# Performance work log

Measured on AMD Instinct MI355X. Metric: run time of the kernel, lower is better.

## Reference

```python
import jax, jax.numpy as jnp
import numpy as np
from jax import lax

N_WORDS = 8192
MAX_WLEN = 16
VOCAB = 500
EMB = 64
HID = 256
N_SENT = 256
SENT_LEN = 32  # N_SENT * SENT_LEN == N_WORDS (sentlens are uniform)


def setup_inputs() -> dict:
    key = jax.random.key(0)
    ks = jax.random.split(key, 12)
    chars = jax.random.randint(ks[0], (N_WORDS, MAX_WLEN), 1, VOCAB, dtype=jnp.int32)
    # packed LSTM requires lengths sorted descending
    wordlens = jnp.sort(jax.random.randint(ks[1], (N_WORDS,), 1, MAX_WLEN + 1, dtype=jnp.int32))[::-1]
    # permutation mapping sorted order -> original order (tensor_unsort input)
    word_orig_idx = jax.random.permutation(ks[2], N_WORDS).astype(jnp.int32)
    emb_table = (jax.random.normal(ks[3], (VOCAB, EMB), dtype=jnp.float32) * 0.1).at[0].set(0.0)  # padding_idx=0
    W_ih = jax.random.normal(ks[4], (4 * HID, EMB), dtype=jnp.float32) * 0.05
    W_hh = jax.random.normal(ks[5], (4 * HID, HID), dtype=jnp.float32) * 0.05
    b_ih = jax.random.normal(ks[6], (4 * HID,), dtype=jnp.float32) * 0.02
    b_hh = jax.random.normal(ks[7], (4 * HID,), dtype=jnp.float32) * 0.02
    attn_w = jax.random.normal(ks[8], (HID,), dtype=jnp.float32) * 0.1  # char_attn weight (zero-init in orig; random for nontrivial test)
    h_init = jax.random.normal(ks[9], (HID,), dtype=jnp.float32) * 0.02  # charlstm_h_init (num_layers=1)
    c_init = jax.random.normal(ks[10], (HID,), dtype=jnp.float32) * 0.02
    return dict(chars=chars, wordlens=wordlens, word_orig_idx=word_orig_idx,
                emb_table=emb_table, W_ih=W_ih, W_hh=W_hh, b_ih=b_ih, b_hh=b_hh,
                attn_w=attn_w, h_init=h_init, c_init=c_init)


def _char_model(chars, wordlens, word_orig_idx, emb_table, W_ih, W_hh, b_ih, b_hh, attn_w, h_init, c_init):
    n = chars.shape[0]
    pad_mask = jnp.arange(MAX_WLEN)[None, :] >= wordlens[:, None]  # [N,L] True where padded
    embs = emb_table[chars]  # [N,L,E] (dropout is identity at eval)

    def step(carry, x_t):
        h, c = carry
        gates = x_t @ W_ih.T + h @ W_hh.T + (b_ih + b_hh)  # [N,4H]
        i, f, g, o = jnp.split(gates, 4, axis=-1)  # torch gate order i,f,g,o
        c = jax.nn.sigmoid(f) * c + jax.nn.sigmoid(i) * jnp.tanh(g)
        h = jax.nn.sigmoid(o) * jnp.tanh(c)
        return (h, c), h

    h0 = jnp.broadcast_to(h_init, (n, HID))
    c0 = jnp.broadcast_to(c_init, (n, HID))
    _, hs = lax.scan(step, (h0, c0), embs.transpose(1, 0, 2))  # hs: [L,N,H]
    char_reps = hs.transpose(1, 0, 2)  # [N,L,H]
    # pad_packed_sequence yields zeros at padded positions
    char_reps = jnp.where(pad_mask[..., None], 0.0, char_reps)
    # masked sigmoid attention pool: weights.bmm(char_reps)
    w = jax.nn.sigmoid(char_reps @ attn_w)  # [N,L]
    w = jnp.where(pad_mask, 0.0, w)
    res = jnp.einsum('nl,nlh->nh', w, char_reps)  # [N,H]
    # tensor_unsort: restore original word order
    res = jnp.zeros_like(res).at[word_orig_idx].set(res)
    # split(sentlens) + pack + pad_packed with uniform sentlens -> reshape
    return res.reshape(N_SENT, SENT_LEN, HID)


def reference(chars, wordlens, word_orig_idx, emb_table, W_ih, W_hh, b_ih, b_hh, attn_w, h_init, c_init):
    return _char_model(chars, wordlens, word_orig_idx, emb_table, W_ih, W_hh, b_ih, b_hh, attn_w, h_init, c_init)
```

## Files before the change

kernel.cpp:

```cpp
#include <hip/hip_runtime.h>
#include <math.h>

#define HID 256
#define EMB 64
#define KTOT 320
#define MT 32
#define NWORDS 8192
#define NBLK (NWORDS / MT)
#define THREADS 512
#define KT 10
#define XSTR 328
#define GSTR 40

typedef _Float16 f16;
typedef _Float16 f16x8 __attribute__((ext_vector_type(8)));
typedef _Float16 f16x4 __attribute__((ext_vector_type(4)));
typedef float f32x4 __attribute__((ext_vector_type(4)));

__device__ __forceinline__ float sigm(float x) { return 1.0f / (1.0f + __expf(-x)); }

__global__ __launch_bounds__(KTOT) void prep_w(const float* __restrict__ W_ih,
                                               const float* __restrict__ W_hh,
                                               const float* __restrict__ b_ih,
                                               const float* __restrict__ b_hh,
                                               f16* __restrict__ Wfrag,
                                               float* __restrict__ bias) {
  const int g = blockIdx.x;
  const int k = threadIdx.x;
  const float w = (k < HID) ? W_hh[g * HID + k] : W_ih[g * EMB + (k - HID)];
  const int kt = k >> 5;
  Wfrag[(size_t)(kt * 1024 + g) * 32 + (k & 31)] = (f16)w;
  if (k == 0) bias[g] = b_ih[g] + b_hh[g];
}

__global__ __launch_bounds__(THREADS, 2) void lstm_mfma(
    const int* __restrict__ chars, const int* __restrict__ wordlens,
    const int* __restrict__ orig_idx, const float* __restrict__ emb_table,
    const float* __restrict__ attn_w, const float* __restrict__ h_init,
    const float* __restrict__ c_init, const f16* __restrict__ Wfrag,
    const float* __restrict__ bias, float* __restrict__ out) {
  __shared__ __align__(16) f16 Xs[MT * XSTR];
  __shared__ __align__(16) f16 gatesS[1024 * GSTR];
  __shared__ int   chars_s[MT * 16];
  __shared__ float part_s[8 * 16];
  __shared__ float wgt_s[MT];
  __shared__ int   len_s[MT];
  __shared__ int   oidx_s[MT];

  const int tid  = threadIdx.x;
  const int w0   = blockIdx.x * MT;
  const int j    = tid & 255;
  const int mh   = tid >> 8;
  const int lane = tid & 63;
  const int wv   = tid >> 6;
  const int r15  = lane & 15, c4 = lane >> 4;
  const int n0   = wv * 128;

  chars_s[tid] = chars[w0 * 16 + tid];
  if (tid < MT) { len_s[tid] = wordlens[w0 + tid]; oidx_s[tid] = orig_idx[w0 + tid]; }

  const float aw   = attn_w[j];
  const float cini = c_init[j];
  const f16   hini = (f16)h_init[j];
#pragma unroll
  for (int mm = 0; mm < 16; ++mm) Xs[(mh * 16 + mm) * XSTR + j] = hini;

  float c_reg[16], res_acc[16], h_new[16];
#pragma unroll
  for (int mm = 0; mm < 16; ++mm) { c_reg[mm] = cini; res_acc[mm] = 0.0f; h_new[mm] = 0.0f; }

  float biasr[8];
#pragma unroll
  for (int ntl = 0; ntl < 8; ++ntl) biasr[ntl] = bias[n0 + ntl * 16 + r15];

  __syncthreads();
  int steps = 1;
#pragma unroll
  for (int m = 0; m < MT; ++m) steps = max(steps, len_s[m]);

  for (int t = 0; t < steps; ++t) {
    {
      const int m = tid >> 4, eg = tid & 15;
      const int ch = chars_s[m * 16 + t];
      const float4 e = ((const float4*)emb_table)[ch * 16 + eg];
      f16x4 ev = { (f16)e.x, (f16)e.y, (f16)e.z, (f16)e.w };
      *(f16x4*)&Xs[m * XSTR + HID + eg * 4] = ev;
    }
    __syncthreads();

    f32x4 acc[8][2];
#pragma unroll
    for (int ntl = 0; ntl < 8; ++ntl) {
      const f32x4 b4 = { biasr[ntl], biasr[ntl], biasr[ntl], biasr[ntl] };
      acc[ntl][0] = b4;
      acc[ntl][1] = b4;
    }

#pragma unroll 2
    for (int kt = 0; kt < KT; ++kt) {
      const f16x8 a0 = *(const f16x8*)&Xs[r15 * XSTR + kt * 32 + c4 * 8];
      const f16x8 a1 = *(const f16x8*)&Xs[(16 + r15) * XSTR + kt * 32 + c4 * 8];
      const f16x8* __restrict__ Wp = (const f16x8*)(Wfrag + (size_t)kt * 1024 * 32);
#pragma unroll
      for (int ntl = 0; ntl < 8; ++ntl) {
        const f16x8 b = Wp[(size_t)(n0 + ntl * 16 + r15) * 4 + c4];
        acc[ntl][0] = __builtin_amdgcn_mfma_f32_16x16x32_f16(a0, b, acc[ntl][0], 0, 0, 0);
        acc[ntl][1] = __builtin_amdgcn_mfma_f32_16x16x32_f16(a1, b, acc[ntl][1], 0, 0, 0);
      }
    }

#pragma unroll
    for (int ntl = 0; ntl < 8; ++ntl) {
      const int g = n0 + ntl * 16 + r15;
#pragma unroll
      for (int mt = 0; mt < 2; ++mt) {
        const f32x4 v = acc[ntl][mt];
        f16x4 hv = { (f16)v.x, (f16)v.y, (f16)v.z, (f16)v.w };
        *(f16x4*)&gatesS[g * GSTR + mt * 16 + c4 * 4] = hv;
      }
    }
    __syncthreads();

    f16x8 gA[4], gB[4];
#pragma unroll
    for (int q = 0; q < 4; ++q) {
      const int g = q * 256 + j;
      gA[q] = *(const f16x8*)&gatesS[g * GSTR + mh * 16];
      gB[q] = *(const f16x8*)&gatesS[g * GSTR + mh * 16 + 8];
    }
#pragma unroll
    for (int mm = 0; mm < 16; ++mm) {
      const float gi = (float)(mm < 8 ? gA[0][mm & 7] : gB[0][mm & 7]);
      const float gf = (float)(mm < 8 ? gA[1][mm & 7] : gB[1][mm & 7]);
      const float gg = (float)(mm < 8 ? gA[2][mm & 7] : gB[2][mm & 7]);
      const float go = (float)(mm < 8 ? gA[3][mm & 7] : gB[3][mm & 7]);
      const float ig = sigm(gi);
      const float fg = sigm(gf);
      const float gv = tanhf(gg);
      const float og = sigm(go);
      const float cc = fg * c_reg[mm] + ig * gv;
      c_reg[mm] = cc;
      h_new[mm] = og * tanhf(cc);
    }
#pragma unroll
    for (int mm = 0; mm < 16; ++mm)
      Xs[(mh * 16 + mm) * XSTR + j] = (f16)h_new[mm];

#pragma unroll
    for (int mm = 0; mm < 16; ++mm) {
      float p = h_new[mm] * aw;
      p += __shfl_xor(p, 1);  p += __shfl_xor(p, 2);  p += __shfl_xor(p, 4);
      p += __shfl_xor(p, 8);  p += __shfl_xor(p, 16); p += __shfl_xor(p, 32);
      if (lane == 0) part_s[wv * 16 + mm] = p;
    }
    __syncthreads();
    if (tid < MT) {
      const int m = tid;
      const int base = (m >> 4) * 4;
      const float s = part_s[(base + 0) * 16 + (m & 15)] + part_s[(base + 1) * 16 + (m & 15)]
                    + part_s[(base + 2) * 16 + (m & 15)] + part_s[(base + 3) * 16 + (m & 15)];
      wgt_s[m] = (t < len_s[m]) ? sigm(s) : 0.0f;
    }
    __syncthreads();
#pragma unroll
    for (int mm = 0; mm < 16; ++mm)
      res_acc[mm] += wgt_s[mh * 16 + mm] * h_new[mm];
  }

#pragma unroll
  for (int mm = 0; mm < 16; ++mm)
    out[(size_t)oidx_s[mh * 16 + mm] * HID + j] = res_acc[mm];
}

extern "C" void kernel_launch(void* const* d_in, const int* in_sizes, int n_in,
                              void* d_out, int out_size, void* d_ws, size_t ws_size,
                              hipStream_t stream) {
  const int*   chars    = (const int*)d_in[0];
  const int*   wordlens = (const int*)d_in[1];
  const int*   orig_idx = (const int*)d_in[2];
  const float* emb      = (const float*)d_in[3];
  const float* W_ih     = (const float*)d_in[4];
  const float* W_hh     = (const float*)d_in[5];
  const float* b_ih     = (const float*)d_in[6];
  const float* b_hh     = (const float*)d_in[7];
  const float* attn_w   = (const float*)d_in[8];
  const float* h_init   = (const float*)d_in[9];
  const float* c_init   = (const float*)d_in[10];
  float* out = (float*)d_out;

  f16*   Wfrag = (f16*)d_ws;
  float* bias  = (float*)((char*)d_ws + (size_t)1024 * 320 * sizeof(f16));
  if (ws_size < (size_t)1024 * 320 * sizeof(f16) + 1024 * sizeof(float)) return;

  hipLaunchKernelGGL(prep_w, dim3(1024), dim3(KTOT), 0, stream,
                     W_ih, W_hh, b_ih, b_hh, Wfrag, bias);
  hipLaunchKernelGGL(lstm_mfma, dim3(NBLK), dim3(THREADS), 0, stream,
                     chars, wordlens, orig_idx, emb, attn_w, h_init, c_init,
                     Wfrag, bias, out);
}
```

Baseline: 289.3 us.

## Interleave gate columns so each lane holds all four gates, drop gates LDS round-trip

Weights are permuted in prep so each wave's 64 output columns hold the i, f, g and o gates for the same 16 hidden units. The cell update then runs directly on MFMA accumulators instead of going through a large gates shared-memory buffer. The block grows to 1024 threads (16 waves), weight fragments are software-prefetched one k-tile ahead, and the next step's embedding load and h write are merged into the post-update phase with lighter barriers. This removes the big LDS staging buffer and one barrier per step, at the cost of more register pressure per thread and a larger block.

```diff
diff --git a/kernel.cpp b/kernel.cpp
--- a/kernel.cpp
+++ b/kernel.cpp
@@ -5,171 +5,203 @@
 #define EMB 64
 #define KTOT 320
 #define MT 32
-#define NWORDS 8192
-#define NBLK (NWORDS / MT)
-#define THREADS 512
+#define NBLK 256
+#define THREADS 1024
 #define KT 10
 #define XSTR 328
-#define GSTR 40
 
 typedef _Float16 f16;
+typedef _Float16 f16x2 __attribute__((ext_vector_type(2)));
 typedef _Float16 f16x8 __attribute__((ext_vector_type(8)));
-typedef _Float16 f16x4 __attribute__((ext_vector_type(4)));
 typedef float f32x4 __attribute__((ext_vector_type(4)));
 
 __device__ __forceinline__ float sigm(float x) { return 1.0f / (1.0f + __expf(-x)); }
+
+__device__ __forceinline__ void bar_lds() {
+  asm volatile("s_waitcnt lgkmcnt(0)" ::: "memory");
+  __builtin_amdgcn_sched_barrier(0);
+  __builtin_amdgcn_s_barrier();
+  __builtin_amdgcn_sched_barrier(0);
+}
 
 __global__ __launch_bounds__(KTOT) void prep_w(const float* __restrict__ W_ih,
                                                const float* __restrict__ W_hh,
                                                const float* __restrict__ b_ih,
                                                const float* __restrict__ b_hh,
                                                f16* __restrict__ Wfrag,
-                                               float* __restrict__ bias) {
+                                               float* __restrict__ bias_p) {
   const int g = blockIdx.x;
   const int k = threadIdx.x;
+  const int q = g >> 8, u = g & 255;
+  const int col = ((u >> 4) << 6) + (q << 4) + (u & 15);
   const float w = (k < HID) ? W_hh[g * HID + k] : W_ih[g * EMB + (k - HID)];
   const int kt = k >> 5;
-  Wfrag[(size_t)(kt * 1024 + g) * 32 + (k & 31)] = (f16)w;
-  if (k == 0) bias[g] = b_ih[g] + b_hh[g];
-}
-
-__global__ __launch_bounds__(THREADS, 2) void lstm_mfma(
+  Wfrag[((size_t)(kt * 1024 + col)) * 32 + (k & 31)] = (f16)w;
+  if (k == 0) bias_p[col] = b_ih[g] + b_hh[g];
+}
+
+__global__ __launch_bounds__(THREADS, 4) void lstm_mfma(
     const int* __restrict__ chars, const int* __restrict__ wordlens,
     const int* __restrict__ orig_idx, const float* __restrict__ emb_table,
     const float* __restrict__ attn_w, const float* __restrict__ h_init,
     const float* __restrict__ c_init, const f16* __restrict__ Wfrag,
-    const float* __restrict__ bias, float* __restrict__ out) {
+    const float* __restrict__ bias_p, float* __restrict__ out) {
   __shared__ __align__(16) f16 Xs[MT * XSTR];
-  __shared__ __align__(16) f16 gatesS[1024 * GSTR];
+  __shared__ float attP[16 * MT];
+  __shared__ float wgt_s[MT];
   __shared__ int   chars_s[MT * 16];
-  __shared__ float part_s[8 * 16];
-  __shared__ float wgt_s[MT];
   __shared__ int   len_s[MT];
   __shared__ int   oidx_s[MT];
 
   const int tid  = threadIdx.x;
   const int w0   = blockIdx.x * MT;
-  const int j    = tid & 255;
-  const int mh   = tid >> 8;
   const int lane = tid & 63;
   const int wv   = tid >> 6;
   const int r15  = lane & 15, c4 = lane >> 4;
-  const int n0   = wv * 128;
-
-  chars_s[tid] = chars[w0 * 16 + tid];
+  const int n0   = wv * 64;
+  const int u    = wv * 16 + r15;
+
+  if (tid < MT * 16) chars_s[tid] = chars[w0 * 16 + tid];
   if (tid < MT) { len_s[tid] = wordlens[w0 + tid]; oidx_s[tid] = orig_idx[w0 + tid]; }
 
-  const float aw   = attn_w[j];
-  const float cini = c_init[j];
-  const f16   hini = (f16)h_init[j];
-#pragma unroll
-  for (int mm = 0; mm < 16; ++mm) Xs[(mh * 16 + mm) * XSTR + j] = hini;
-
-  float c_reg[16], res_acc[16], h_new[16];
-#pragma unroll
-  for (int mm = 0; mm < 16; ++mm) { c_reg[mm] = cini; res_acc[mm] = 0.0f; h_new[mm] = 0.0f; }
-
-  float biasr[8];
-#pragma unroll
-  for (int ntl = 0; ntl < 8; ++ntl) biasr[ntl] = bias[n0 + ntl * 16 + r15];
+  {
+    const int j = tid & 255, mb = tid >> 8;
+    const f16 hv = (f16)h_init[j];
+#pragma unroll
+    for (int mm = 0; mm < 8; ++mm) Xs[(mb + mm * 4) * XSTR + j] = hv;
+  }
+  {
+    const int m = tid >> 5, e2 = tid & 31;
+    const int ch = chars_s[m * 16 + 0];
+    const int ch_g = chars[(w0 + m) * 16 + 0];
+    (void)ch;
+    const float2 e = ((const float2*)emb_table)[ch_g * 32 + e2];
+    f16x2 ev = { (f16)e.x, (f16)e.y };
+    *(f16x2*)&Xs[m * XSTR + HID + e2 * 2] = ev;
+  }
+
+  const float aw = attn_w[u];
+  float biasr[4];
+#pragma unroll
+  for (int q = 0; q < 4; ++q) biasr[q] = bias_p[n0 + q * 16 + r15];
+
+  float c_reg[8], res[8], h_new[8];
+  {
+    const float cini = c_init[u];
+#pragma unroll
+    for (int i = 0; i < 8; ++i) { c_reg[i] = cini; res[i] = 0.0f; h_new[i] = 0.0f; }
+  }
 
   __syncthreads();
+
   int steps = 1;
 #pragma unroll
   for (int m = 0; m < MT; ++m) steps = max(steps, len_s[m]);
 
+  const size_t bofs = (size_t)(n0 + r15) * 4 + c4;
+  f16x8 bc[4];
+#pragma unroll
+  for (int q = 0; q < 4; ++q)
+    bc[q] = ((const f16x8*)Wfrag)[bofs + (size_t)q * 64];
+
   for (int t = 0; t < steps; ++t) {
-    {
-      const int m = tid >> 4, eg = tid & 15;
-      const int ch = chars_s[m * 16 + t];
-      const float4 e = ((const float4*)emb_table)[ch * 16 + eg];
-      f16x4 ev = { (f16)e.x, (f16)e.y, (f16)e.z, (f16)e.w };
-      *(f16x4*)&Xs[m * XSTR + HID + eg * 4] = ev;
-    }
-    __syncthreads();
-
-    f32x4 acc[8][2];
-#pragma unroll
-    for (int ntl = 0; ntl < 8; ++ntl) {
-      const f32x4 b4 = { biasr[ntl], biasr[ntl], biasr[ntl], biasr[ntl] };
-      acc[ntl][0] = b4;
-      acc[ntl][1] = b4;
-    }
-
-#pragma unroll 2
+    f32x4 acc[4][2];
+#pragma unroll
+    for (int q = 0; q < 4; ++q) {
+      const f32x4 b4 = { biasr[q], biasr[q], biasr[q], biasr[q] };
+      acc[q][0] = b4; acc[q][1] = b4;
+    }
+
+#pragma unroll
     for (int kt = 0; kt < KT; ++kt) {
+      const int ktn = (kt + 1 < KT) ? kt + 1 : 0;
+      f16x8 bn[4];
+      const f16x8* __restrict__ Wn = ((const f16x8*)Wfrag) + (size_t)ktn * 4096;
+#pragma unroll
+      for (int q = 0; q < 4; ++q) bn[q] = Wn[bofs + (size_t)q * 64];
+
       const f16x8 a0 = *(const f16x8*)&Xs[r15 * XSTR + kt * 32 + c4 * 8];
       const f16x8 a1 = *(const f16x8*)&Xs[(16 + r15) * XSTR + kt * 32 + c4 * 8];
-      const f16x8* __restrict__ Wp = (const f16x8*)(Wfrag + (size_t)kt * 1024 * 32);
-#pragma unroll
-      for (int ntl = 0; ntl < 8; ++ntl) {
-        const f16x8 b = Wp[(size_t)(n0 + ntl * 16 + r15) * 4 + c4];
-        acc[ntl][0] = __builtin_amdgcn_mfma_f32_16x16x32_f16(a0, b, acc[ntl][0], 0, 0, 0);
-        acc[ntl][1] = __builtin_amdgcn_mfma_f32_16x16x32_f16(a1, b, acc[ntl][1], 0, 0, 0);
-      }
-    }
-
-#pragma unroll
-    for (int ntl = 0; ntl < 8; ++ntl) {
-      const int g = n0 + ntl * 16 + r15;
-#pragma unroll
-      for (int mt = 0; mt < 2; ++mt) {
-        const f32x4 v = acc[ntl][mt];
-        f16x4 hv = { (f16)v.x, (f16)v.y, (f16)v.z, (f16)v.w };
-        *(f16x4*)&gatesS[g * GSTR + mt * 16 + c4 * 4] = hv;
-      }
-    }
-    __syncthreads();
-
-    f16x8 gA[4], gB[4];
-#pragma unroll
-    for (int q = 0; q < 4; ++q) {
-      const int g = q * 256 + j;
-      gA[q] = *(const f16x8*)&gatesS[g * GSTR + mh * 16];
-      gB[q] = *(const f16x8*)&gatesS[g * GSTR + mh * 16 + 8];
-    }
-#pragma unroll
-    for (int mm = 0; mm < 16; ++mm) {
-      const float gi = (float)(mm < 8 ? gA[0][mm & 7] : gB[0][mm & 7]);
-      const float gf = (float)(mm < 8 ? gA[1][mm & 7] : gB[1][mm & 7]);
-      const float gg = (float)(mm < 8 ? gA[2][mm & 7] : gB[2][mm & 7]);
-      const float go = (float)(mm < 8 ? gA[3][mm & 7] : gB[3][mm & 7]);
-      const float ig = sigm(gi);
-      const float fg = sigm(gf);
-      const float gv = tanhf(gg);
-      const float og = sigm(go);
-      const float cc = fg * c_reg[mm] + ig * gv;
-      c_reg[mm] = cc;
-      h_new[mm] = og * tanhf(cc);
-    }
-#pragma unroll
-    for (int mm = 0; mm < 16; ++mm)
-      Xs[(mh * 16 + mm) * XSTR + j] = (f16)h_new[mm];
-
-#pragma unroll
-    for (int mm = 0; mm < 16; ++mm) {
-      float p = h_new[mm] * aw;
-      p += __shfl_xor(p, 1);  p += __shfl_xor(p, 2);  p += __shfl_xor(p, 4);
-      p += __shfl_xor(p, 8);  p += __shfl_xor(p, 16); p += __shfl_xor(p, 32);
-      if (lane == 0) part_s[wv * 16 + mm] = p;
-    }
-    __syncthreads();
+#pragma unroll
+      for (int q = 0; q < 4; ++q) {
+        acc[q][0] = __builtin_amdgcn_mfma_f32_16x16x32_f16(a0, bc[q], acc[q][0], 0, 0, 0);
+        acc[q][1] = __builtin_amdgcn_mfma_f32_16x16x32_f16(a1, bc[q], acc[q][1], 0, 0, 0);
+      }
+#pragma unroll
+      for (int q = 0; q < 4; ++q) bc[q] = bn[q];
+    }
+
+#pragma unroll
+    for (int mt = 0; mt < 2; ++mt) {
+#pragma unroll
+      for (int r = 0; r < 4; ++r) {
+        const int idx = mt * 4 + r;
+        const float gi = acc[0][mt][r];
+        const float gf = acc[1][mt][r];
+        const float gg = acc[2][mt][r];
+        const float go = acc[3][mt][r];
+        const float cc = sigm(gf) * c_reg[idx] + sigm(gi) * tanhf(gg);
+        c_reg[idx] = cc;
+        h_new[idx] = sigm(go) * tanhf(cc);
+      }
+    }
+
+    bar_lds();
+
+    if (t + 1 < steps) {
+#pragma unroll
+      for (int mt = 0; mt < 2; ++mt)
+#pragma unroll
+        for (int r = 0; r < 4; ++r)
+          Xs[(mt * 16 + c4 * 4 + r) * XSTR + u] = (f16)h_new[mt * 4 + r];
+      {
+        const int m = tid >> 5, e2 = tid & 31;
+        const int ch = chars_s[m * 16 + (t + 1)];
+        const float2 e = ((const float2*)emb_table)[ch * 32 + e2];
+        f16x2 ev = { (f16)e.x, (f16)e.y };
+        *(f16x2*)&Xs[m * XSTR + HID + e2 * 2] = ev;
+      }
+    }
+
+#pragma unroll
+    for (int mt = 0; mt < 2; ++mt) {
+#pragma unroll
+      for (int r = 0; r < 4; ++r) {
+        const int idx = mt * 4 + r;
+        float p = h_new[idx] * aw;
+        p += __shfl_xor(p, 1); p += __shfl_xor(p, 2);
+        p += __shfl_xor(p, 4); p += __shfl_xor(p, 8);
+        if (r15 == 0) attP[wv * MT + mt * 16 + c4 * 4 + r] = p;
+      }
+    }
+
+    bar_lds();
+
     if (tid < MT) {
-      const int m = tid;
-      const int base = (m >> 4) * 4;
-      const float s = part_s[(base + 0) * 16 + (m & 15)] + part_s[(base + 1) * 16 + (m & 15)]
-                    + part_s[(base + 2) * 16 + (m & 15)] + part_s[(base + 3) * 16 + (m & 15)];
-      wgt_s[m] = (t < len_s[m]) ? sigm(s) : 0.0f;
-    }
-    __syncthreads();
-#pragma unroll
-    for (int mm = 0; mm < 16; ++mm)
-      res_acc[mm] += wgt_s[mh * 16 + mm] * h_new[mm];
-  }
-
-#pragma unroll
-  for (int mm = 0; mm < 16; ++mm)
-    out[(size_t)oidx_s[mh * 16 + mm] * HID + j] = res_acc[mm];
+      float s = 0.0f;
+#pragma unroll
+      for (int w = 0; w < 16; ++w) s += attP[w * MT + tid];
+      wgt_s[tid] = (t < len_s[tid]) ? sigm(s) : 0.0f;
+    }
+
+    bar_lds();
+
+#pragma unroll
+    for (int mt = 0; mt < 2; ++mt)
+#pragma unroll
+      for (int r = 0; r < 4; ++r) {
+        const int idx = mt * 4 + r;
+        res[idx] += wgt_s[mt * 16 + c4 * 4 + r] * h_new[idx];
+      }
+  }
+
+#pragma unroll
+  for (int mt = 0; mt < 2; ++mt)
+#pragma unroll
+    for (int r = 0; r < 4; ++r) {
+      const int m = mt * 16 + c4 * 4 + r;
+      out[(size_t)oidx_s[m] * HID + u] = res[mt * 4 + r];
+    }
 }
 
 extern "C" void kernel_launch(void* const* d_in, const int* in_sizes, int n_in,
@@ -188,13 +220,13 @@
   const float* c_init   = (const float*)d_in[10];
   float* out = (float*)d_out;
 
-  f16*   Wfrag = (f16*)d_ws;
-  float* bias  = (float*)((char*)d_ws + (size_t)1024 * 320 * sizeof(f16));
-  if (ws_size < (size_t)1024 * 320 * sizeof(f16) + 1024 * sizeof(float)) return;
+  f16*   Wfrag  = (f16*)d_ws;
+  float* bias_p = (float*)((char*)d_ws + (size_t)KTOT * 1024 * sizeof(f16));
+  if (ws_size < (size_t)KTOT * 1024 * sizeof(f16) + 1024 * sizeof(float)) return;
 
   hipLaunchKernelGGL(prep_w, dim3(1024), dim3(KTOT), 0, stream,
-                     W_ih, W_hh, b_ih, b_hh, Wfrag, bias);
+                     W_ih, W_hh, b_ih, b_hh, Wfrag, bias_p);
   hipLaunchKernelGGL(lstm_mfma, dim3(NBLK), dim3(THREADS), 0, stream,
                      chars, wordlens, orig_idx, emb, attn_w, h_init, c_init,
-                     Wfrag, bias, out);
-}
+                     Wfrag, bias_p, out);
+}
```

Result: slower. 351.8 us (+21.6%).
